# Kernel optimization log

Hardware: AMD Instinct MI355X
Metric: run time of the kernel (lower is better)

## Reference

```python
import itertools
import jax
import jax.numpy as jnp
from jax import lax
import numpy as np

R = 256            # resolution
F = 128            # feature_size
D = 2              # dimensions (len(grid_min))
NUM_LEVELS = 8     # log2(R)
IGNORE_LEVELS = 2
LEVELS_USED = NUM_LEVELS - IGNORE_LEVELS  # 6
GRID_MIN = -1.0
GRID_MAX = 1.0
N_PTS = 262144


def gaussian_kernel(M, std):
    # matches scipy.signal.gaussian(M, std), normalized to sum 1
    n = np.arange(M, dtype=np.float64) - (M - 1) / 2.0
    w = np.exp(-0.5 * (n / std) ** 2)
    return (w / w.sum()).astype(np.float32)


def conv1d_same(x, kern, axis):
    # 'same'-mode convolution along `axis`; kern is symmetric so corr == conv
    M = kern.shape[0]
    x = jnp.moveaxis(x, axis, -1)
    shp = x.shape
    xr = x.reshape(-1, 1, shp[-1])  # (B, C=1, L)
    y = lax.conv_general_dilated(
        xr, kern[None, None, :].astype(x.dtype), (1,),
        [(M // 2, (M - 1) // 2)], dimension_numbers=('NCH', 'OIH', 'NCH'))
    return jnp.moveaxis(y.reshape(shp), -1, axis)


def downsample(base, s):
    # Gaussian blur with window s (std=s/2) along each spatial dim,
    # reflect-pad by s, conv 'same', crop back -> same-resolution blur pyramid
    kern = jnp.asarray(gaussian_kernel(s, s / 2.0))
    x = base
    for dim in range(D):
        pad = [(s, s) if d == dim else (0, 0) for d in range(x.ndim)]
        x = jnp.pad(x, pad, mode='reflect')
        x = conv1d_same(x, kern, dim)
        x = lax.slice_in_dim(x, s, R + s, axis=dim)
    return x


def setup_inputs() -> dict:
    key = jax.random.key(0)
    ks = jax.random.split(key, 5)
    pt = jax.random.uniform(ks[0], (N_PTS, D), jnp.float32,
                            minval=GRID_MIN, maxval=GRID_MAX)
    base_features = jax.random.normal(ks[1], (R, R, F), jnp.float32) * 0.1
    b_levels = jnp.full((LEVELS_USED,), 1.0 / LEVELS_USED, jnp.float32)
    W1 = jax.random.normal(ks[2], (F, 128), jnp.float32) / np.sqrt(F)
    b1 = jnp.zeros((128,), jnp.float32)
    W2 = jax.random.normal(ks[3], (128, 4), jnp.float32) / np.sqrt(128.0)
    b2 = jnp.zeros((4,), jnp.float32)
    return {"pt": pt, "base_features": base_features, "b_levels": b_levels,
            "W1": W1, "b1": b1, "W2": W2, "b2": b2}


def _mipmap_features(pt, base_features, b_levels):
    alpha = (pt - GRID_MIN) / (GRID_MAX - GRID_MIN)          # (N, D)
    idx_f = alpha * (R - 1.0)
    idx = idx_f.astype(jnp.int32)
    frac = idx_f - idx.astype(idx_f.dtype)                    # jnp.modf frac part
    fused = jnp.zeros((pt.shape[0], F), dtype=pt.dtype)
    for lvl in range(LEVELS_USED):
        mip = base_features if lvl == 0 else downsample(base_features, 2 ** lvl)
        feat = jnp.zeros_like(fused)
        # 2^D corner gather + multilinear interpolation (vectorized over N)
        for corner in itertools.product((0, 1), repeat=D):
            xi = tuple(jnp.clip(idx[:, d] + corner[d], 0, R - 1)
                       for d in range(D))
            w = jnp.ones((pt.shape[0],), dtype=pt.dtype)
            for d in range(D):
                w = w * (frac[:, d] if corner[d] else (1.0 - frac[:, d]))
            feat = feat + mip[xi] * w[:, None]
        fused = fused + feat * b_levels[lvl]
    return fused


def reference(pt, base_features, b_levels, W1, b1, W2, b2):
    fused = _mipmap_features(pt, base_features, b_levels)     # (N, F)
    h = jax.nn.relu(fused @ W1 + b1)
    return h @ W2 + b2                                        # (N, 4)
```

## Files before the change

kernel.cpp:

```cpp
#include <hip/hip_runtime.h>


typedef short short8 __attribute__((ext_vector_type(8)));
typedef float f32x4 __attribute__((ext_vector_type(4)));
typedef unsigned int u32x4 __attribute__((ext_vector_type(4)));

__device__ __forceinline__ unsigned short f2bfbits(float f) {
    unsigned int x = __float_as_uint(f);
    x += 0x7fffu + ((x >> 16) & 1u);
    return (unsigned short)(x >> 16);
}

__device__ __forceinline__ float bflo(unsigned int u) {
    return __uint_as_float(u << 16);
}

__device__ __forceinline__ float bfhi(unsigned int u) {
    return __uint_as_float(u & 0xffff0000u);
}

__global__ void kcoef(const float* blev, float* coef) {
    if (blockIdx.x != 0 || threadIdx.x != 0) return;
    int offs[6];
    offs[0] = 0; offs[1] = 0; offs[2] = 2; offs[3] = 6; offs[4] = 14; offs[5] = 30;
    for (int l = 1; l <= 5; l++) {
        int s = 1 << l;
        int off = offs[l];
        float sum = 0.0f;
        for (int m = 0; m < s; m++) {
            float x = ((float)m - (float)(s - 1) * 0.5f) / ((float)s * 0.5f);
            float w = expf(-0.5f * x * x);
            coef[off + m] = w;
            sum += w;
        }
        float bl = blev[l];
        for (int m = 0; m < s; m++) {
            float w = coef[off + m] / sum;
            coef[off + m] = w;
            coef[64 + off + m] = w * bl;
        }
    }
    coef[128] = blev[0];
}

__global__ void kconvW(const float* W1, unsigned short* W1T) {
    int i = blockIdx.x * 256 + threadIdx.x;
    int k = i >> 7;
    int n = i & 127;
    W1T[n * 128 + k] = f2bfbits(W1[i]);
}

__global__ void kgemm(const float* base, const unsigned short* W1T,
                      float* G0p) {
    __shared__ float stg[64 * 132];
    int tid = threadIdx.x;
    int wv = tid >> 6;
    int lane = tid & 63;
    int colI = lane & 15;
    int quad = lane >> 4;
    int m0 = blockIdx.x * 64 + wv * 16;
    f32x4 zero = {0.0f, 0.0f, 0.0f, 0.0f};
    f32x4 acc0 = zero; f32x4 acc1 = zero; f32x4 acc2 = zero; f32x4 acc3 = zero;
    f32x4 acc4 = zero; f32x4 acc5 = zero; f32x4 acc6 = zero; f32x4 acc7 = zero;
    for (int kc = 0; kc < 4; kc++) {
        int k0 = kc * 32 + quad * 8;
        const float* ap = base + (size_t)(m0 + colI) * 128 + k0;
        f32x4 af0 = *(const f32x4*)(ap);
        f32x4 af1 = *(const f32x4*)(ap + 4);
        short8 a;
        a[0] = (short)f2bfbits(af0[0]); a[1] = (short)f2bfbits(af0[1]);
        a[2] = (short)f2bfbits(af0[2]); a[3] = (short)f2bfbits(af0[3]);
        a[4] = (short)f2bfbits(af1[0]); a[5] = (short)f2bfbits(af1[1]);
        a[6] = (short)f2bfbits(af1[2]); a[7] = (short)f2bfbits(af1[3]);
        const unsigned short* wb = W1T + (size_t)colI * 128 + k0;
        short8 b0 = *(const short8*)(wb + 0 * 16 * 128);
        short8 b1 = *(const short8*)(wb + 1 * 16 * 128);
        short8 b2 = *(const short8*)(wb + 2 * 16 * 128);
        short8 b3 = *(const short8*)(wb + 3 * 16 * 128);
        short8 b4 = *(const short8*)(wb + 4 * 16 * 128);
        short8 b5 = *(const short8*)(wb + 5 * 16 * 128);
        short8 b6 = *(const short8*)(wb + 6 * 16 * 128);
        short8 b7 = *(const short8*)(wb + 7 * 16 * 128);
        acc0 = __builtin_amdgcn_mfma_f32_16x16x32_bf16(a, b0, acc0, 0, 0, 0);
        acc1 = __builtin_amdgcn_mfma_f32_16x16x32_bf16(a, b1, acc1, 0, 0, 0);
        acc2 = __builtin_amdgcn_mfma_f32_16x16x32_bf16(a, b2, acc2, 0, 0, 0);
        acc3 = __builtin_amdgcn_mfma_f32_16x16x32_bf16(a, b3, acc3, 0, 0, 0);
        acc4 = __builtin_amdgcn_mfma_f32_16x16x32_bf16(a, b4, acc4, 0, 0, 0);
        acc5 = __builtin_amdgcn_mfma_f32_16x16x32_bf16(a, b5, acc5, 0, 0, 0);
        acc6 = __builtin_amdgcn_mfma_f32_16x16x32_bf16(a, b6, acc6, 0, 0, 0);
        acc7 = __builtin_amdgcn_mfma_f32_16x16x32_bf16(a, b7, acc7, 0, 0, 0);
    }
    int mlb = (wv * 16 + quad * 4) * 2;
#define STG(c, A) { int n = c * 16 + colI; \
    float* p = stg + (n >> 1) * 132 + mlb + (n & 1); \
    p[0] = A[0]; p[2] = A[1]; p[4] = A[2]; p[6] = A[3]; }
    STG(0, acc0) STG(1, acc1) STG(2, acc2) STG(3, acc3)
    STG(4, acc4) STG(5, acc5) STG(6, acc6) STG(7, acc7)
#undef STG
    __syncthreads();
    size_t m0b2 = (size_t)blockIdx.x * 128;
    for (int j = tid; j < 2048; j += 256) {
        int fp = j >> 5;
        int q = (j & 31) * 4;
        f32x4 v = *(const f32x4*)&stg[fp * 132 + q];
        *(f32x4*)(G0p + (size_t)fp * 131072 + m0b2 + q) = v;
    }
}

__device__ void blur_level(const float* in_t, float* H_t,
                           const float* kh_s, const float* kv_s,
                           int tid, float* acc, int S, int off) {
    int half = S / 2;
    int nrows = 31 + S;
    for (int g = tid; g < nrows * 8; g += 512) {
        int yy = (16 - half) + (g >> 3);
        int xg = g & 7;
        float a00 = 0.0f, a01 = 0.0f, a10 = 0.0f, a11 = 0.0f;
        float a20 = 0.0f, a21 = 0.0f, a30 = 0.0f, a31 = 0.0f;
        int cb = xg * 4 + 16 - half;
        for (int t = 0; t < S + 3; t++) {
            float v0 = in_t[(yy * 66 + cb + t) * 2 + 0];
            float v1 = in_t[(yy * 66 + cb + t) * 2 + 1];
            if (t < S)              { float k = kh_s[off + t];     a00 += k * v0; a01 += k * v1; }
            if (t >= 1 && t - 1 < S){ float k = kh_s[off + t - 1]; a10 += k * v0; a11 += k * v1; }
            if (t >= 2 && t - 2 < S){ float k = kh_s[off + t - 2]; a20 += k * v0; a21 += k * v1; }
            if (t >= 3 && t - 3 < S){ float k = kh_s[off + t - 3]; a30 += k * v0; a31 += k * v1; }
        }
        int hb = (yy * 33 + xg * 4) * 2;
        H_t[hb + 0] = a00; H_t[hb + 1] = a01;
        H_t[hb + 2] = a10; H_t[hb + 3] = a11;
        H_t[hb + 4] = a20; H_t[hb + 5] = a21;
        H_t[hb + 6] = a30; H_t[hb + 7] = a31;
    }
    __syncthreads();
    int xl = tid & 31;
    int ygrp = tid >> 5;
    int ybase = ygrp * 2 + 16 - half;
    for (int t = 0; t <= S; t++) {
        float h0 = H_t[((ybase + t) * 33 + xl) * 2 + 0];
        float h1 = H_t[((ybase + t) * 33 + xl) * 2 + 1];
        if (t < S)  { float k = kv_s[off + t];     acc[0] += k * h0; acc[1] += k * h1; }
        if (t >= 1) { float k = kv_s[off + t - 1]; acc[2] += k * h0; acc[3] += k * h1; }
    }
    __syncthreads();
}

__global__ void kblur(const float* G0p, const float* coef, float* Gb) {
    __shared__ float in_t[63 * 66 * 2];
    __shared__ float H_t[63 * 33 * 2];
    __shared__ float kh_s[64];
    __shared__ float kv_s[64];
    __shared__ float b0s[1];
    int tid = threadIdx.x;
    int bid = blockIdx.x;
    int xcd = bid & 7;
    int q = bid >> 3;
    int fp = (xcd << 3) | (q >> 6);
    int s = q & 63;
    int x0 = (s & 7) * 32;
    int y0 = (s >> 3) * 32;
    const float* Pin = G0p + (size_t)fp * 131072;
    float* Pout = Gb + (size_t)fp * 131072;
    if (tid < 64) { kh_s[tid] = coef[tid]; kv_s[tid] = coef[64 + tid]; }
    if (tid == 64) b0s[0] = coef[128];
    for (int i = tid; i < 63 * 63; i += 512) {
        int yy = i / 63;
        int xx = i - yy * 63;
        int gy = y0 + yy - 16; if (gy < 0) gy = -gy; if (gy > 255) gy = 510 - gy;
        int gx = x0 + xx - 16; if (gx < 0) gx = -gx; if (gx > 255) gx = 510 - gx;
        const float* src = Pin + (size_t)(gy * 256 + gx) * 2;
        in_t[(yy * 66 + xx) * 2 + 0] = src[0];
        in_t[(yy * 66 + xx) * 2 + 1] = src[1];
    }
    __syncthreads();
    int xl = tid & 31;
    int ygrp = tid >> 5;
    float acc[4];
    float b0 = b0s[0];
    acc[0] = b0 * in_t[((ygrp * 2 + 16) * 66 + xl + 16) * 2 + 0];
    acc[1] = b0 * in_t[((ygrp * 2 + 16) * 66 + xl + 16) * 2 + 1];
    acc[2] = b0 * in_t[((ygrp * 2 + 17) * 66 + xl + 16) * 2 + 0];
    acc[3] = b0 * in_t[((ygrp * 2 + 17) * 66 + xl + 16) * 2 + 1];
    blur_level(in_t, H_t, kh_s, kv_s, tid, acc, 2, 0);
    blur_level(in_t, H_t, kh_s, kv_s, tid, acc, 4, 2);
    blur_level(in_t, H_t, kh_s, kv_s, tid, acc, 8, 6);
    blur_level(in_t, H_t, kh_s, kv_s, tid, acc, 16, 14);
    blur_level(in_t, H_t, kh_s, kv_s, tid, acc, 32, 30);
    for (int i = 0; i < 2; i++) {
        int gy = y0 + ygrp * 2 + i;
        int gx = x0 + xl;
        float* dst = Pout + (size_t)(gy * 256 + gx) * 2;
        dst[0] = acc[i * 2 + 0];
        dst[1] = acc[i * 2 + 1];
    }
}

__global__ void ktrans(const float* Gb, unsigned int* G2) {
    __shared__ unsigned int lds[32 * 65];
    int t = threadIdx.x;
    int x0 = blockIdx.x * 32;
    int y = blockIdx.y;
    int base = y * 256 + x0;
    int fp = t >> 2;
    int p0 = (t & 3) * 8;
    const float* src = Gb + ((size_t)fp * 65536 + base + p0) * 2;
    for (int k4 = 0; k4 < 4; k4++) {
        f32x4 v = *(const f32x4*)(src + k4 * 4);
        unsigned int u0 = ((unsigned int)f2bfbits(v[1]) << 16)
                        | (unsigned int)f2bfbits(v[0]);
        unsigned int u1 = ((unsigned int)f2bfbits(v[3]) << 16)
                        | (unsigned int)f2bfbits(v[2]);
        lds[(p0 + k4 * 2 + 0) * 65 + fp] = u0;
        lds[(p0 + k4 * 2 + 1) * 65 + fp] = u1;
    }
    __syncthreads();
    int px = t >> 3;
    int f0 = (t & 7) * 8;
    u32x4 o0, o1;
    o0[0] = lds[px * 65 + f0 + 0]; o0[1] = lds[px * 65 + f0 + 1];
    o0[2] = lds[px * 65 + f0 + 2]; o0[3] = lds[px * 65 + f0 + 3];
    o1[0] = lds[px * 65 + f0 + 4]; o1[1] = lds[px * 65 + f0 + 5];
    o1[2] = lds[px * 65 + f0 + 6]; o1[3] = lds[px * 65 + f0 + 7];
    unsigned int* dst = G2 + (size_t)(base + px) * 64 + f0;
    *(u32x4*)(dst) = o0;
    *(u32x4*)(dst + 4) = o1;
}

__global__ void kgather(const float* pt, const unsigned int* G2,
                        const float* b1, const float* W2, const float* b2,
                        float* out) {
    int lane = threadIdx.x & 63;
    int wv = threadIdx.x >> 6;
    int i = blockIdx.x * 4 + wv;
    float py = pt[2 * i];
    float px = pt[2 * i + 1];
    float ay = (py + 1.0f) * 0.5f * 255.0f;
    float ax = (px + 1.0f) * 0.5f * 255.0f;
    int iy = (int)ay;
    int ix = (int)ax;
    if (iy < 0) iy = 0;
    if (iy > 255) iy = 255;
    if (ix < 0) ix = 0;
    if (ix > 255) ix = 255;
    float fy = ay - (float)iy;
    float fx = ax - (float)ix;
    int iy1 = iy + 1; if (iy1 > 255) iy1 = 255;
    int ix1 = ix + 1; if (ix1 > 255) ix1 = 255;
    float w00 = (1.0f - fy) * (1.0f - fx);
    float w01 = (1.0f - fy) * fx;
    float w10 = fy * (1.0f - fx);
    float w11 = fy * fx;
    int f = lane * 2;
    unsigned int u00 = G2[(iy  * 256 + ix ) * 64 + lane];
    unsigned int u01 = G2[(iy  * 256 + ix1) * 64 + lane];
    unsigned int u10 = G2[(iy1 * 256 + ix ) * 64 + lane];
    unsigned int u11 = G2[(iy1 * 256 + ix1) * 64 + lane];
    float v0 = w00 * bflo(u00) + w01 * bflo(u01)
             + w10 * bflo(u10) + w11 * bflo(u11) + b1[f];
    float v1 = w00 * bfhi(u00) + w01 * bfhi(u01)
             + w10 * bfhi(u10) + w11 * bfhi(u11) + b1[f + 1];
    if (v0 < 0.0f) v0 = 0.0f;
    if (v1 < 0.0f) v1 = 0.0f;
    float o0 = v0 * W2[f * 4 + 0] + v1 * W2[f * 4 + 4];
    float o1 = v0 * W2[f * 4 + 1] + v1 * W2[f * 4 + 5];
    float o2 = v0 * W2[f * 4 + 2] + v1 * W2[f * 4 + 6];
    float o3 = v0 * W2[f * 4 + 3] + v1 * W2[f * 4 + 7];
    for (int m = 32; m >= 1; m >>= 1) {
        o0 += __shfl_xor(o0, m);
        o1 += __shfl_xor(o1, m);
        o2 += __shfl_xor(o2, m);
        o3 += __shfl_xor(o3, m);
    }
    if (lane == 0) {
        out[4 * i + 0] = o0 + b2[0];
        out[4 * i + 1] = o1 + b2[1];
        out[4 * i + 2] = o2 + b2[2];
        out[4 * i + 3] = o3 + b2[3];
    }
}

extern "C" void kernel_launch(void* const* d_in, const int* in_sizes, int n_in,
                              void* d_out, int out_size, void* d_ws, size_t ws_size,
                              hipStream_t stream) {
    const float* pt   = (const float*)d_in[0];
    const float* base = (const float*)d_in[1];
    const float* blev = (const float*)d_in[2];
    const float* W1   = (const float*)d_in[3];
    const float* b1   = (const float*)d_in[4];
    const float* W2   = (const float*)d_in[5];
    const float* b2   = (const float*)d_in[6];
    if (n_in == 7) {
        for (int i = 0; i < 7; i++) {
            int sz = in_sizes[i];
            if (sz == 524288)       pt   = (const float*)d_in[i];
            else if (sz == 8388608) base = (const float*)d_in[i];
            else if (sz == 6)       blev = (const float*)d_in[i];
            else if (sz == 16384)   W1   = (const float*)d_in[i];
            else if (sz == 128)     b1   = (const float*)d_in[i];
            else if (sz == 512)     W2   = (const float*)d_in[i];
            else if (sz == 4)       b2   = (const float*)d_in[i];
        }
    }
    float* out = (float*)d_out;
    char* ws = (char*)d_ws;

    size_t off0 = 1024;
    size_t off1 = off0 + 65536;
    size_t off2 = off1 + 33554432;
    size_t off3 = off2 + 33554432;
    size_t need = off3 + 16777216;
    if (ws_size < need) return;

    float* coef = (float*)ws;
    unsigned short* W1T = (unsigned short*)(ws + off0);
    float* G0p = (float*)(ws + off1);
    float* Gb  = (float*)(ws + off2);
    unsigned int* G2 = (unsigned int*)(ws + off3);

    kcoef<<<1, 64, 0, stream>>>(blev, coef);
    kconvW<<<64, 256, 0, stream>>>(W1, W1T);
    kgemm<<<1024, 256, 0, stream>>>(base, W1T, G0p);
    kblur<<<4096, 512, 0, stream>>>(G0p, coef, Gb);
    ktrans<<<dim3(8, 256), 256, 0, stream>>>(Gb, G2);
    kgather<<<65536, 256, 0, stream>>>(pt, G2, b1, W2, b2, out);
}
```

Baseline: 335.4 us.

## Pack blur tile as bf16 pairs in LDS, split H planes, add nontemporal memory ops

The blur kernel's shared input tile now holds bf16-packed feature pairs in one 32-bit word per pixel, halving LDS footprint and load count. The horizontal-pass buffer is split into two float planes with a padded stride to change bank access patterns. Global stores of intermediates and the transpose kernel's loads become nontemporal to avoid polluting cache, and output stores are vectorized as float2. Rounding the blur input to bf16 before filtering adds precision loss, though the data is later converted to bf16 anyway.

```diff
diff --git a/kernel.cpp b/kernel.cpp
--- a/kernel.cpp
+++ b/kernel.cpp
@@ -3,6 +3,7 @@
 
 typedef short short8 __attribute__((ext_vector_type(8)));
 typedef float f32x4 __attribute__((ext_vector_type(4)));
+typedef float f32x2 __attribute__((ext_vector_type(2)));
 typedef unsigned int u32x4 __attribute__((ext_vector_type(4)));
 
 __device__ __forceinline__ unsigned short f2bfbits(float f) {
@@ -103,11 +104,12 @@
         int fp = j >> 5;
         int q = (j & 31) * 4;
         f32x4 v = *(const f32x4*)&stg[fp * 132 + q];
-        *(f32x4*)(G0p + (size_t)fp * 131072 + m0b2 + q) = v;
-    }
-}
-
-__device__ void blur_level(const float* in_t, float* H_t,
+        __builtin_nontemporal_store(v,
+            (f32x4*)(G0p + (size_t)fp * 131072 + m0b2 + q));
+    }
+}
+
+__device__ void blur_level(const unsigned int* in_t, float* H0, float* H1,
                            const float* kh_s, const float* kv_s,
                            int tid, float* acc, int S, int off) {
     int half = S / 2;
@@ -119,26 +121,28 @@
         float a20 = 0.0f, a21 = 0.0f, a30 = 0.0f, a31 = 0.0f;
         int cb = xg * 4 + 16 - half;
         for (int t = 0; t < S + 3; t++) {
-            float v0 = in_t[(yy * 66 + cb + t) * 2 + 0];
-            float v1 = in_t[(yy * 66 + cb + t) * 2 + 1];
+            unsigned int u = in_t[yy * 67 + cb + t];
+            float v0 = bflo(u);
+            float v1 = bfhi(u);
             if (t < S)              { float k = kh_s[off + t];     a00 += k * v0; a01 += k * v1; }
             if (t >= 1 && t - 1 < S){ float k = kh_s[off + t - 1]; a10 += k * v0; a11 += k * v1; }
             if (t >= 2 && t - 2 < S){ float k = kh_s[off + t - 2]; a20 += k * v0; a21 += k * v1; }
             if (t >= 3 && t - 3 < S){ float k = kh_s[off + t - 3]; a30 += k * v0; a31 += k * v1; }
         }
-        int hb = (yy * 33 + xg * 4) * 2;
-        H_t[hb + 0] = a00; H_t[hb + 1] = a01;
-        H_t[hb + 2] = a10; H_t[hb + 3] = a11;
-        H_t[hb + 4] = a20; H_t[hb + 5] = a21;
-        H_t[hb + 6] = a30; H_t[hb + 7] = a31;
+        int hb = yy * 35 + xg * 4;
+        H0[hb + 0] = a00; H1[hb + 0] = a01;
+        H0[hb + 1] = a10; H1[hb + 1] = a11;
+        H0[hb + 2] = a20; H1[hb + 2] = a21;
+        H0[hb + 3] = a30; H1[hb + 3] = a31;
     }
     __syncthreads();
     int xl = tid & 31;
     int ygrp = tid >> 5;
     int ybase = ygrp * 2 + 16 - half;
     for (int t = 0; t <= S; t++) {
-        float h0 = H_t[((ybase + t) * 33 + xl) * 2 + 0];
-        float h1 = H_t[((ybase + t) * 33 + xl) * 2 + 1];
+        int hi = (ybase + t) * 35 + xl;
+        float h0 = H0[hi];
+        float h1 = H1[hi];
         if (t < S)  { float k = kv_s[off + t];     acc[0] += k * h0; acc[1] += k * h1; }
         if (t >= 1) { float k = kv_s[off + t - 1]; acc[2] += k * h0; acc[3] += k * h1; }
     }
@@ -146,8 +150,9 @@
 }
 
 __global__ void kblur(const float* G0p, const float* coef, float* Gb) {
-    __shared__ float in_t[63 * 66 * 2];
-    __shared__ float H_t[63 * 33 * 2];
+    __shared__ unsigned int in_t[63 * 67];
+    __shared__ float H0s[63 * 35];
+    __shared__ float H1s[63 * 35];
     __shared__ float kh_s[64];
     __shared__ float kv_s[64];
     __shared__ float b0s[1];
@@ -169,29 +174,33 @@
         int gy = y0 + yy - 16; if (gy < 0) gy = -gy; if (gy > 255) gy = 510 - gy;
         int gx = x0 + xx - 16; if (gx < 0) gx = -gx; if (gx > 255) gx = 510 - gx;
         const float* src = Pin + (size_t)(gy * 256 + gx) * 2;
-        in_t[(yy * 66 + xx) * 2 + 0] = src[0];
-        in_t[(yy * 66 + xx) * 2 + 1] = src[1];
+        in_t[yy * 67 + xx] = ((unsigned int)f2bfbits(src[1]) << 16)
+                           | (unsigned int)f2bfbits(src[0]);
     }
     __syncthreads();
     int xl = tid & 31;
     int ygrp = tid >> 5;
     float acc[4];
     float b0 = b0s[0];
-    acc[0] = b0 * in_t[((ygrp * 2 + 16) * 66 + xl + 16) * 2 + 0];
-    acc[1] = b0 * in_t[((ygrp * 2 + 16) * 66 + xl + 16) * 2 + 1];
-    acc[2] = b0 * in_t[((ygrp * 2 + 17) * 66 + xl + 16) * 2 + 0];
-    acc[3] = b0 * in_t[((ygrp * 2 + 17) * 66 + xl + 16) * 2 + 1];
-    blur_level(in_t, H_t, kh_s, kv_s, tid, acc, 2, 0);
-    blur_level(in_t, H_t, kh_s, kv_s, tid, acc, 4, 2);
-    blur_level(in_t, H_t, kh_s, kv_s, tid, acc, 8, 6);
-    blur_level(in_t, H_t, kh_s, kv_s, tid, acc, 16, 14);
-    blur_level(in_t, H_t, kh_s, kv_s, tid, acc, 32, 30);
+    unsigned int uc0 = in_t[(ygrp * 2 + 16) * 67 + xl + 16];
+    unsigned int uc1 = in_t[(ygrp * 2 + 17) * 67 + xl + 16];
+    acc[0] = b0 * bflo(uc0);
+    acc[1] = b0 * bfhi(uc0);
+    acc[2] = b0 * bflo(uc1);
+    acc[3] = b0 * bfhi(uc1);
+    blur_level(in_t, H0s, H1s, kh_s, kv_s, tid, acc, 2, 0);
+    blur_level(in_t, H0s, H1s, kh_s, kv_s, tid, acc, 4, 2);
+    blur_level(in_t, H0s, H1s, kh_s, kv_s, tid, acc, 8, 6);
+    blur_level(in_t, H0s, H1s, kh_s, kv_s, tid, acc, 16, 14);
+    blur_level(in_t, H0s, H1s, kh_s, kv_s, tid, acc, 32, 30);
     for (int i = 0; i < 2; i++) {
         int gy = y0 + ygrp * 2 + i;
         int gx = x0 + xl;
-        float* dst = Pout + (size_t)(gy * 256 + gx) * 2;
-        dst[0] = acc[i * 2 + 0];
-        dst[1] = acc[i * 2 + 1];
+        f32x2 v;
+        v[0] = acc[i * 2 + 0];
+        v[1] = acc[i * 2 + 1];
+        __builtin_nontemporal_store(v,
+            (f32x2*)(Pout + (size_t)(gy * 256 + gx) * 2));
     }
 }
 
@@ -205,7 +214,7 @@
     int p0 = (t & 3) * 8;
     const float* src = Gb + ((size_t)fp * 65536 + base + p0) * 2;
     for (int k4 = 0; k4 < 4; k4++) {
-        f32x4 v = *(const f32x4*)(src + k4 * 4);
+        f32x4 v = __builtin_nontemporal_load((const f32x4*)(src + k4 * 4));
         unsigned int u0 = ((unsigned int)f2bfbits(v[1]) << 16)
                         | (unsigned int)f2bfbits(v[0]);
         unsigned int u1 = ((unsigned int)f2bfbits(v[3]) << 16)
```

After: 553.0 us. +64.9%, slower.
